# Performance work log

Hardware: AMD Instinct MI355X
Metric: run time of the kernel (lower is better)

## Reference

```python
import jax, jax.numpy as jnp
import numpy as np
import math

B, N, K = 16, 1024, 16
NODE_DIM, MSG = 32, 128
EDGE_DIM = 4
EIN = MSG + EDGE_DIM  # edge_input_dim = message_dim + edge_dim
EPS = 1e-8
PI = math.pi


def _knn(pts, k):
    # pairwise_distance_etaphi + topk(smallest) -> neighbor indices [B,N,K]
    eta, phi = pts[:, 0], pts[:, 1]                                  # [B,N]
    deta = eta[:, :, None] - eta[:, None, :]
    dphi = jnp.mod(phi[:, :, None] - phi[:, None, :] + PI, 2 * PI) - PI
    dist = deta ** 2 + dphi ** 2                                     # [B,N,N]
    _, idx = jax.lax.top_k(-dist, k)                                 # smallest-k, sorted
    return idx


def _gather(x, idx):
    # x: [B,C,N], idx: [B,N,K] -> neighbor features [B,C,N,K]
    return jnp.take_along_axis(x[:, :, None, :], idx[:, None, :, :], axis=3)


def _ptrapphi(x):
    px, py, pz, e = x[:, 0:1], x[:, 1:2], x[:, 2:3], x[:, 3:4]
    pt = jnp.sqrt(px ** 2 + py ** 2)
    rap = 0.5 * jnp.log1p(2.0 * pz / jnp.clip(e - pz, 1e-20))
    phi = jnp.arctan2(py, px)
    return pt, rap, phi


def _pairwise_lv_fts(xi, xj):
    # [lnkt, lnz, lndelta, lnm2] along channel dim
    pti, rapi, phii = _ptrapphi(xi)
    ptj, rapj, phij = _ptrapphi(xj)
    ptmin = jnp.minimum(pti, ptj)
    dphi = jnp.mod(phii - phij + PI, 2 * PI) - PI
    delta = jnp.sqrt((rapi - rapj) ** 2 + dphi ** 2)
    lndelta = jnp.log(jnp.clip(delta, EPS))
    lnkt = jnp.log(jnp.clip(ptmin * delta, EPS))
    lnz = jnp.log(jnp.clip(ptmin / jnp.clip(pti + ptj, EPS), EPS))
    xij = xi + xj
    m2 = jnp.clip(xij[:, 3:4] ** 2 - (xij[:, :3] ** 2).sum(1, keepdims=True), EPS)
    lnm2 = jnp.log(m2)
    return jnp.concatenate([lnkt, lnz, lndelta, lnm2], axis=1)


def _bn(x, s, b):
    # eval-mode BatchNorm folded into per-channel scale/bias
    sh = (1, -1) + (1,) * (x.ndim - 2)
    return x * s.reshape(sh) + b.reshape(sh)


def _conv1x1(w, x):
    return jnp.einsum('oc,bc...->bo...', w, x)


def setup_inputs():
    key = jax.random.key(0)
    ks = jax.random.split(key, 12)
    pts = jax.random.normal(ks[0], (B, 2, N), jnp.float32)
    fts = jax.random.normal(ks[1], (B, NODE_DIM, N), jnp.float32)
    p3 = jax.random.normal(ks[2], (B, 3, N), jnp.float32) * 5.0
    e = jnp.sqrt((p3 ** 2).sum(1, keepdims=True) + 0.5)  # physical 4-vectors (E > |p|)
    lvs = jnp.concatenate([p3, e], axis=1)
    mask = jax.random.bernoulli(ks[3], 0.9, (B, 1, N))
    w = lambda k, o, i: (jax.random.normal(k, (o, i), jnp.float32) / np.sqrt(i)).astype(jnp.float32)
    return dict(
        pts=pts, fts=fts, lvs=lvs, mask=mask,
        bn1_s=jnp.ones(NODE_DIM, jnp.float32), bn1_b=jnp.zeros(NODE_DIM, jnp.float32),
        w_node=w(ks[4], MSG // 2, NODE_DIM),
        bn2_s=jnp.ones(EIN, jnp.float32), bn2_b=jnp.zeros(EIN, jnp.float32),
        w_e1=w(ks[5], MSG, EIN),
        bn3_s=jnp.ones(MSG, jnp.float32), bn3_b=jnp.zeros(MSG, jnp.float32),
        w_e2=w(ks[6], MSG, MSG),
        se_w1=w(ks[7], MSG // 16, MSG),
        se_w2=w(ks[8], MSG, MSG // 16),
    )


def reference(pts, fts, lvs, mask, bn1_s, bn1_b, w_node, bn2_s, bn2_b, w_e1, bn3_s, bn3_b, w_e2, se_w1, se_w2):
    idx = _knn(pts, K)                                                  # [B,N,K]
    # node_encode: BN -> ReLU -> 1x1 conv (node_dim -> MSG//2)
    node = _conv1x1(w_node, jax.nn.relu(_bn(fts, bn1_s, bn1_b)))        # [B,MSG/2,N]
    node_ngb = _gather(node, idx)                                       # [B,MSG/2,N,K]
    node_ctr = jnp.broadcast_to(node[..., None], node_ngb.shape)
    lvs_ngb = _gather(lvs, idx)                                         # [B,4,N,K]
    lv_fts = _pairwise_lv_fts(jnp.broadcast_to(lvs[..., None], lvs_ngb.shape), lvs_ngb)
    mf = mask.astype(jnp.float32)
    valid = _gather(mf, idx) * mf[..., None]                            # [B,1,N,K]
    x = jnp.concatenate([node_ctr, node_ngb, lv_fts], axis=1)           # [B,EIN,N,K]
    # edge_mlp: BN-ReLU-Conv1x1 x2
    x = _conv1x1(w_e1, jax.nn.relu(_bn(x, bn2_s, bn2_b)))
    x = _conv1x1(w_e2, jax.nn.relu(_bn(x, bn3_s, bn3_b)))               # [B,MSG,N,K]
    # SqueezeAndExcitation2d over valid edges
    n = valid.sum((2, 3))
    n = jnp.where(n == 0, 1.0, n)                                       # [B,1]
    y = (x * valid).sum((2, 3)) / n                                     # [B,MSG]
    y = jax.nn.sigmoid(jax.nn.relu(y @ se_w1.T) @ se_w2.T)
    x = x * y[:, :, None, None]
    # masked mean aggregation over neighbors
    x = x * valid
    agg = x.sum(-1) / jnp.clip(valid.sum(-1), 1.0)                      # [B,MSG,N]
    return agg
```

## Files before the change

kernel.cpp:

```cpp
#include <hip/hip_runtime.h>
#include <hip/hip_bf16.h>
#include <math.h>

typedef unsigned short u16;
typedef unsigned long long u64;

#define BB 16
#define NN 1024
#define KK 16
#define MSG 128
#define EINC 132
#define EPSF 1e-8f
#define PIF 3.14159274101257324f
#define TWOPIF 6.28318548202514648f

__device__ __forceinline__ float bf2f(u16 u) {
    return __uint_as_float(((unsigned int)u) << 16);
}
__device__ __forceinline__ float ldf(const void* p, int i, int fdt) {
    return fdt ? ((const float*)p)[i] : bf2f(((const u16*)p)[i]);
}
__device__ __forceinline__ float4 ldf4(const void* p, int i, int fdt) {
    if (fdt) return ((const float4*)p)[i >> 2];
    ushort4 u = ((const ushort4*)p)[i >> 2];
    return make_float4(bf2f(u.x), bf2f(u.y), bf2f(u.z), bf2f(u.w));
}
__device__ __forceinline__ float maskval(const void* m, int i, int mode) {
    if (mode == 0) return bf2f(((const u16*)m)[i]);
    if (mode == 1) return ((const float*)m)[i];
    if (mode == 2) return ((const unsigned char*)m)[i] ? 1.f : 0.f;
    return ((const int*)m)[i] ? 1.f : 0.f;
}

__global__ void sniff_kernel(const unsigned int* __restrict__ bn1s,
                             const u16* __restrict__ mask,
                             int* __restrict__ ctl) {
    if (threadIdx.x == 0 && blockIdx.x == 0) {
        ctl[0] = (bn1s[0] == 0x3F800000u) ? 1 : 0;
        bool bf = false, f32 = false, i8 = false;
        for (int q = 0; q < 64; ++q) {
            u16 u = mask[q];
            if (u == 0x3F80u) { if ((q & 1) == 0) bf = true; else f32 = true; }
            if (u == 0x0101u) i8 = true;
        }
        ctl[1] = bf ? 0 : (f32 ? 1 : (i8 ? 2 : 3));
    }
}

__device__ __forceinline__ float wrap2pi(float dp) {
    if (dp >= TWOPIF) dp = __fsub_rn(dp, TWOPIF);
    if (dp < 0.f) dp = __fadd_rn(dp, TWOPIF);
    return dp;
}

__device__ __forceinline__ void sort16(u64* x) {
#pragma unroll
    for (int k = 2; k <= 16; k <<= 1)
#pragma unroll
        for (int j = k >> 1; j > 0; j >>= 1)
#pragma unroll
            for (int i = 0; i < 16; ++i) {
                int l = i ^ j;
                if (l > i) {
                    bool up = ((i & k) == 0);
                    bool lt = x[l] < x[i];
                    bool sw = up ? lt : !lt;
                    u64 a = sw ? x[l] : x[i];
                    u64 b = sw ? x[i] : x[l];
                    x[i] = a; x[l] = b;
                }
            }
}

__device__ __forceinline__ void merge16(u64* L, const u64* R) {
#pragma unroll
    for (int k = 0; k < 16; ++k) {
        u64 o = R[15 - k];
        L[k] = (o < L[k]) ? o : L[k];
    }
#pragma unroll
    for (int j = 8; j > 0; j >>= 1)
#pragma unroll
        for (int i = 0; i < 16; ++i) {
            int l = i ^ j;
            if (l > i) {
                bool sw = L[l] < L[i];
                u64 a = sw ? L[l] : L[i];
                u64 b = sw ? L[i] : L[l];
                L[i] = a; L[l] = b;
            }
        }
}

__global__ __launch_bounds__(256) void knn_kernel(const void* __restrict__ pts,
                                                  int* __restrict__ idx,
                                                  const int* __restrict__ ctl) {
    __shared__ __align__(16) char smem[24672];
    float* seL = (float*)smem;
    float* spL = seL + 1092;
    float* pdL = (float*)smem;
    u16*   piL = (u16*)(smem + 16448);
    int fdt = ctl[0];
    int blk = blockIdx.x;
    int b = blk >> 6;
    int ibase = (blk & 63) << 4;
    int t = threadIdx.x;
    int pb = b * 2 * NN;
    for (int j = t; j < NN; j += 256) {
        int a = (j >> 6) * 68 + (j & 63);
        seL[a] = ldf(pts, pb + j, fdt);
        spL[a] = ldf(pts, pb + NN + j, fdt);
    }
    __syncthreads();
    int p = t >> 4, s = t & 15;
    u64 lst[16];
    {
        int i = ibase + p;
        int ia = (i >> 6) * 68 + (i & 63);
        float ei = seL[ia], pii = spL[ia];
        u64 grp[16];
#pragma unroll
        for (int g = 0; g < 4; ++g) {
            const float* sep = &seL[s * 68 + g * 16];
            const float* spp = &spL[s * 68 + g * 16];
            int jb = (s << 6) + (g << 4);
#pragma unroll
            for (int q4 = 0; q4 < 4; ++q4) {
                float4 e4 = *(const float4*)(sep + 4 * q4);
                float4 p4 = *(const float4*)(spp + 4 * q4);
                float ee[4] = { e4.x, e4.y, e4.z, e4.w };
                float pp[4] = { p4.x, p4.y, p4.z, p4.w };
#pragma unroll
                for (int q = 0; q < 4; ++q) {
                    float de = __fsub_rn(ei, ee[q]);
                    float dp = wrap2pi(__fadd_rn(__fsub_rn(pii, pp[q]), PIF));
                    float dphi = __fsub_rn(dp, PIF);
                    float cd = __fadd_rn(__fmul_rn(de, de), __fmul_rn(dphi, dphi));
                    grp[q4 * 4 + q] = ((u64)__float_as_uint(cd) << 10)
                                      | (unsigned)(jb + q4 * 4 + q);
                }
            }
            sort16(grp);
            if (g == 0) {
#pragma unroll
                for (int k = 0; k < 16; ++k) lst[k] = grp[k];
            } else {
                merge16(lst, grp);
            }
        }
    }
    __syncthreads();
    {
        int base = p * 257 + s * 16;
#pragma unroll
        for (int k = 0; k < 16; ++k) {
            pdL[base + k] = __uint_as_float((unsigned)(lst[k] >> 10));
            piL[base + k] = (u16)(lst[k] & 1023u);
        }
    }
    for (int stg = 0; stg < 4; ++stg) {
        __syncthreads();
        int stride = 8 >> stg;
        if (s < stride) {
            int Lb = p * 257 + s * 16;
            int Rb = p * 257 + (s + stride) * 16;
            u64 L[16], R[16];
#pragma unroll
            for (int k = 0; k < 16; ++k)
                L[k] = ((u64)__float_as_uint(pdL[Lb + k]) << 10) | piL[Lb + k];
#pragma unroll
            for (int k = 0; k < 16; ++k)
                R[k] = ((u64)__float_as_uint(pdL[Rb + k]) << 10) | piL[Rb + k];
            merge16(L, R);
#pragma unroll
            for (int k = 0; k < 16; ++k) {
                pdL[Lb + k] = __uint_as_float((unsigned)(L[k] >> 10));
                piL[Lb + k] = (u16)(L[k] & 1023u);
            }
        }
    }
    __syncthreads();
    {
        int p2 = t >> 4, k2 = t & 15;
        idx[(b * NN + ibase + p2) * KK + k2] = (int)piL[p2 * 257 + k2];
    }
}

__global__ __launch_bounds__(256) void ab1_kernel(
    const void* __restrict__ fts, const void* __restrict__ lvs,
    const void* __restrict__ bn1_s, const void* __restrict__ bn1_b,
    const void* __restrict__ w_node,
    const void* __restrict__ bn2_s, const void* __restrict__ bn2_b,
    float* __restrict__ rAB, float* __restrict__ prpx,
    const int* __restrict__ ctl) {
    __shared__ __align__(16) float fL[32 * 36];
    __shared__ __align__(16) float wnL[64 * 36];
    __shared__ float s2L[128], b2L[128];
    int fdt = ctl[0];
    int blk = blockIdx.x;
    int b = blk >> 5;
    int ibase = (blk & 31) << 5;
    int t = threadIdx.x;
    {
        int c = t >> 3, q = t & 7;
        float s1c = ldf(bn1_s, c, fdt), b1c = ldf(bn1_b, c, fdt);
        float4 v = ldf4(fts, (b * 32 + c) * NN + ibase + q * 4, fdt);
        float vv[4] = { v.x, v.y, v.z, v.w };
#pragma unroll
        for (int j = 0; j < 4; ++j)
            fL[(q * 4 + j) * 36 + c] = fmaxf(vv[j] * s1c + b1c, 0.f);
    }
#pragma unroll
    for (int m = 0; m < 2; ++m) {
        int e = t * 2 + m;
        int o = e >> 3, q = e & 7;
        float4 w = ldf4(w_node, o * 32 + q * 4, fdt);
        float* d = &wnL[o * 36 + q * 4];
        d[0] = w.x; d[1] = w.y; d[2] = w.z; d[3] = w.w;
    }
    if (t < 128) { s2L[t] = ldf(bn2_s, t, fdt); b2L[t] = ldf(bn2_b, t, fdt); }
    if (t < 32) {
        int i = ibase + t;
        int lb = b * 4 * NN;
        float px = ldf(lvs, lb + i, fdt),          py = ldf(lvs, lb + NN + i, fdt);
        float pz = ldf(lvs, lb + 2 * NN + i, fdt), e  = ldf(lvs, lb + 3 * NN + i, fdt);
        float pt = sqrtf(px * px + py * py);
        float rr = 2.f * pz / fmaxf(e - pz, 1e-20f);
        rr = fmaxf(rr, -0.99999994f);
        float rap = 0.5f * log1pf(rr);
        float phi = atan2f(py, px);
        float* o = prpx + (size_t)(b * NN + i) * 8;
        o[0] = px; o[1] = py; o[2] = pz; o[3] = e;
        o[4] = pt; o[5] = rap; o[6] = phi; o[7] = 0.f;
    }
    __syncthreads();
    int p = t >> 3, og = t & 7;
    float fr[32];
#pragma unroll
    for (int cc = 0; cc < 32; cc += 4) {
        float4 v = *(const float4*)&fL[p * 36 + cc];
        fr[cc] = v.x; fr[cc + 1] = v.y; fr[cc + 2] = v.z; fr[cc + 3] = v.w;
    }
    float aa[8];
#pragma unroll
    for (int m = 0; m < 8; ++m) {
        int no = og * 8 + m;
        float a = 0.f;
#pragma unroll
        for (int cc = 0; cc < 32; cc += 4) {
            float4 w = *(const float4*)&wnL[no * 36 + cc];
            a += w.x * fr[cc] + w.y * fr[cc + 1] + w.z * fr[cc + 2] + w.w * fr[cc + 3];
        }
        aa[m] = a;
    }
    size_t base = (size_t)(b * NN + ibase + p) * 128 + og * 8;
    float lo[8], hi[8];
#pragma unroll
    for (int m = 0; m < 8; ++m) {
        int no = og * 8 + m;
        lo[m] = fmaxf(aa[m] * s2L[no] + b2L[no], 0.f);
        hi[m] = fmaxf(aa[m] * s2L[64 + no] + b2L[64 + no], 0.f);
    }
    *(float4*)(rAB + base)      = make_float4(lo[0], lo[1], lo[2], lo[3]);
    *(float4*)(rAB + base + 4)  = make_float4(lo[4], lo[5], lo[6], lo[7]);
    *(float4*)(rAB + base + 64) = make_float4(hi[0], hi[1], hi[2], hi[3]);
    *(float4*)(rAB + base + 68) = make_float4(hi[4], hi[5], hi[6], hi[7]);
}

__global__ __launch_bounds__(256) void ab2_kernel(
    const float* __restrict__ rAB, const void* __restrict__ w_e1,
    float* __restrict__ A, float* __restrict__ Bv,
    const int* __restrict__ ctl) {
    __shared__ float rT[64 * 68];
    __shared__ float wsh[2048];
    int fdt = ctl[0];
    int blk = blockIdx.x;
    int half = blk & 1;
    int pc = blk >> 1;
    int b = pc >> 4, i0 = (pc & 15) << 6;
    int t = threadIdx.x;
    {
        int r = t >> 2, q = t & 3;
        const float4* src = (const float4*)(rAB + (size_t)(b * NN + i0 + r) * 128
                                            + half * 64 + q * 16);
#pragma unroll
        for (int m = 0; m < 4; ++m) {
            float4 v = src[m];
            int c = q * 16 + 4 * m;
            rT[(c + 0) * 68 + r] = v.x; rT[(c + 1) * 68 + r] = v.y;
            rT[(c + 2) * 68 + r] = v.z; rT[(c + 3) * 68 + r] = v.w;
        }
    }
    float acc[8][4];
#pragma unroll
    for (int oi = 0; oi < 8; ++oi)
#pragma unroll
        for (int ci = 0; ci < 4; ++ci) acc[oi][ci] = 0.f;
    int og = t >> 4, cg = t & 15;
    for (int jt = 0; jt < 4; ++jt) {
        __syncthreads();
        {
            int o = t >> 1, jh = (t & 1) * 8;
            float4 wa = ldf4(w_e1, o * EINC + half * 64 + jt * 16 + jh, fdt);
            float4 wb = ldf4(w_e1, o * EINC + half * 64 + jt * 16 + jh + 4, fdt);
            wsh[(jh + 0) * 128 + o] = wa.x; wsh[(jh + 1) * 128 + o] = wa.y;
            wsh[(jh + 2) * 128 + o] = wa.z; wsh[(jh + 3) * 128 + o] = wa.w;
            wsh[(jh + 4) * 128 + o] = wb.x; wsh[(jh + 5) * 128 + o] = wb.y;
            wsh[(jh + 6) * 128 + o] = wb.z; wsh[(jh + 7) * 128 + o] = wb.w;
        }
        __syncthreads();
#pragma unroll
        for (int jj = 0; jj < 16; ++jj) {
            int c = jt * 16 + jj;
            float4 hv = *(const float4*)&rT[c * 68 + cg * 4];
            float4 w0 = *(const float4*)&wsh[jj * 128 + og * 8];
            float4 w1 = *(const float4*)&wsh[jj * 128 + og * 8 + 4];
            float wv[8] = { w0.x, w0.y, w0.z, w0.w, w1.x, w1.y, w1.z, w1.w };
            float hvv[4] = { hv.x, hv.y, hv.z, hv.w };
#pragma unroll
            for (int oi = 0; oi < 8; ++oi)
#pragma unroll
                for (int ci = 0; ci < 4; ++ci)
                    acc[oi][ci] += wv[oi] * hvv[ci];
        }
    }
    float* dst = half ? Bv : A;
#pragma unroll
    for (int ci = 0; ci < 4; ++ci) {
        size_t g = (size_t)(b * NN + i0 + cg * 4 + ci) * 128 + og * 8;
        *(float4*)(dst + g)     = make_float4(acc[0][ci], acc[1][ci], acc[2][ci], acc[3][ci]);
        *(float4*)(dst + g + 4) = make_float4(acc[4][ci], acc[5][ci], acc[6][ci], acc[7][ci]);
    }
}

__global__ __launch_bounds__(256) void edge_kernel(
    const void* __restrict__ mask, const int* __restrict__ idx,
    const float* __restrict__ A, const float* __restrict__ Bv,
    const float* __restrict__ prpx,
    const void* __restrict__ bn2_s, const void* __restrict__ bn2_b,
    const void* __restrict__ w_e1,
    const void* __restrict__ bn3_s, const void* __restrict__ bn3_b,
    float* __restrict__ Hs, float* __restrict__ cnt, float* __restrict__ Thp,
    const int* __restrict__ ctl) {
    __shared__ float rlvL[128 * 4];
    __shared__ float validL[128];
    __shared__ int   idxsL[128];
    __shared__ float thL[128 * 5];
    int fdt = ctl[0], mmode = ctl[1];
    int blk = blockIdx.x;
    int b = blk >> 7;
    int pbase = (blk & 127) << 3;
    int t = threadIdx.x;

    if (t < 128) {
        int col = t, pt = col >> 4, k = col & 15;
        int i = pbase + pt;
        int jn = idx[(b * NN + i) * KK + k];
        idxsL[col] = jn;
        float mi = maskval(mask, b * NN + i, mmode);
        float mj = maskval(mask, b * NN + jn, mmode);
        validL[col] = (mi != 0.f && mj != 0.f) ? 1.f : 0.f;
        const float4* pc = (const float4*)(prpx + (size_t)(b * NN + i) * 8);
        const float4* pn = (const float4*)(prpx + (size_t)(b * NN + jn) * 8);
        float4 c0 = pc[0], c1 = pc[1], n0 = pn[0], n1 = pn[1];
        float ptmin = fminf(c1.x, n1.x);
        float dpr = (c1.z - n1.z) + PIF;
        float r = fmodf(dpr, TWOPIF);
        r = (r < 0.f) ? r + TWOPIF : r;
        float dphi = r - PIF;
        float dr = c1.y - n1.y;
        float delta = sqrtf(dr * dr + dphi * dphi);
        float lndelta = logf(fmaxf(delta, EPSF));
        float lnkt = logf(fmaxf(ptmin * delta, EPSF));
        float lnz = logf(fmaxf(ptmin / fmaxf(c1.x + n1.x, EPSF), EPSF));
        float sx = c0.x + n0.x, sy = c0.y + n0.y, sz = c0.z + n0.z, see = c0.w + n0.w;
        float m2 = fmaxf(see * see - (sx * sx + sy * sy + sz * sz), EPSF);
        float f4a[4] = { lnkt, lnz, lndelta, logf(m2) };
        float rv[4];
#pragma unroll
        for (int q = 0; q < 4; ++q)
            rv[q] = fmaxf(f4a[q] * ldf(bn2_s, MSG + q, fdt) + ldf(bn2_b, MSG + q, fdt), 0.f);
        *(float4*)&rlvL[col * 4] = make_float4(rv[0], rv[1], rv[2], rv[3]);
    }
    __syncthreads();
    int pt = t >> 5, cq = t & 31;
    int i = pbase + pt;
    int c0 = cq * 4;
    float4 a4 = *(const float4*)(A + (size_t)(b * NN + i) * 128 + c0);
    float4 s3 = ldf4(bn3_s, c0, fdt), b3 = ldf4(bn3_b, c0, fdt);
    float4 w0 = ldf4(w_e1, (c0 + 0) * EINC + 128, fdt);
    float4 w1 = ldf4(w_e1, (c0 + 1) * EINC + 128, fdt);
    float4 w2 = ldf4(w_e1, (c0 + 2) * EINC + 128, fdt);
    float4 w3 = ldf4(w_e1, (c0 + 3) * EINC + 128, fdt);
    float4 acc = make_float4(0.f, 0.f, 0.f, 0.f);
#pragma unroll
    for (int k = 0; k < 16; ++k) {
        int col = pt * 16 + k;
        int jn = idxsL[col];
        float vk = validL[col];
        float4 rl = *(const float4*)&rlvL[col * 4];
        float4 b4 = *(const float4*)(Bv + (size_t)(b * NN + jn) * 128 + c0);
        float e0 = a4.x + b4.x + w0.x * rl.x + w0.y * rl.y + w0.z * rl.z + w0.w * rl.w;
        float e1 = a4.y + b4.y + w1.x * rl.x + w1.y * rl.y + w1.z * rl.z + w1.w * rl.w;
        float e2 = a4.z + b4.z + w2.x * rl.x + w2.y * rl.y + w2.z * rl.z + w2.w * rl.w;
        float e3 = a4.w + b4.w + w3.x * rl.x + w3.y * rl.y + w3.z * rl.z + w3.w * rl.w;
        acc.x += vk * fmaxf(s3.x * e0 + b3.x, 0.f);
        acc.y += vk * fmaxf(s3.y * e1 + b3.y, 0.f);
        acc.z += vk * fmaxf(s3.z * e2 + b3.z, 0.f);
        acc.w += vk * fmaxf(s3.w * e3 + b3.w, 0.f);
    }
    *(float4*)(Hs + (size_t)(b * NN + i) * 128 + c0) = acc;
    float4 a2;
    a2.x = acc.x + __shfl_down(acc.x, 32, 64);
    a2.y = acc.y + __shfl_down(acc.y, 32, 64);
    a2.z = acc.z + __shfl_down(acc.z, 32, 64);
    a2.w = acc.w + __shfl_down(acc.w, 32, 64);
    int wv_ = t >> 6;
    if ((t & 63) < 32) {
        thL[(cq * 4 + 0) * 5 + wv_] = a2.x;
        thL[(cq * 4 + 1) * 5 + wv_] = a2.y;
        thL[(cq * 4 + 2) * 5 + wv_] = a2.z;
        thL[(cq * 4 + 3) * 5 + wv_] = a2.w;
    }
    if (t < 8) {
        float cs = 0.f;
#pragma unroll
        for (int k = 0; k < 16; ++k) cs += validL[t * 16 + k];
        cnt[b * NN + pbase + t] = cs;
    }
    __syncthreads();
    if (t < 128)
        Thp[(size_t)blk * 128 + t] = thL[t * 5 + 0] + thL[t * 5 + 1]
                                   + thL[t * 5 + 2] + thL[t * 5 + 3];
}

__global__ __launch_bounds__(128) void se_kernel(const float* __restrict__ Thp,
                                                 const float* __restrict__ cnt,
                                                 const void* __restrict__ w_e2,
                                                 const void* __restrict__ se_w1,
                                                 const void* __restrict__ se_w2,
                                                 float* __restrict__ y,
                                                 const int* __restrict__ ctl) {
    int b = blockIdx.x, t = threadIdx.x;
    int fdt = ctl[0];
    __shared__ float ThL[128], ybar[MSG], hh[8], part[2];
    float a = 0.f;
    for (int m = t; m < NN; m += 128) a += cnt[b * NN + m];
#pragma unroll
    for (int off = 32; off; off >>= 1) a += __shfl_down(a, off, 64);
    if ((t & 63) == 0) part[t >> 6] = a;
    float tv = 0.f;
    for (int p = 0; p < 128; ++p) tv += Thp[(size_t)(b * 128 + p) * 128 + t];
    ThL[t] = tv;
    __syncthreads();
    float n = part[0] + part[1];
    n = (n == 0.f) ? 1.f : n;
    float T = 0.f;
#pragma unroll
    for (int j4 = 0; j4 < 32; ++j4) {
        float4 w = ldf4(w_e2, t * MSG + j4 * 4, fdt);
        T += w.x * ThL[j4 * 4] + w.y * ThL[j4 * 4 + 1] +
             w.z * ThL[j4 * 4 + 2] + w.w * ThL[j4 * 4 + 3];
    }
    ybar[t] = T / n;
    __syncthreads();
    if (t < 8) {
        float s = 0.f;
        for (int c = 0; c < MSG; ++c) s += ybar[c] * ldf(se_w1, t * MSG + c, fdt);
        hh[t] = fmaxf(s, 0.f);
    }
    __syncthreads();
    float s = 0.f;
#pragma unroll
    for (int j = 0; j < 8; ++j) s += hh[j] * ldf(se_w2, t * 8 + j, fdt);
    y[b * MSG + t] = 1.f / (1.f + expf(-s));
}

__global__ __launch_bounds__(256) void fin_kernel(const float* __restrict__ Hs,
                                                  const float* __restrict__ cnt,
                                                  const float* __restrict__ y,
                                                  const void* __restrict__ w_e2,
                                                  void* __restrict__ out,
                                                  const int* __restrict__ ctl) {
    __shared__ float HsT[128 * 68];
    __shared__ float wsh[16 * 64];
    __shared__ float yL[64], icL[64];
    int fdt = ctl[0];
    int blk = blockIdx.x;
    int oh = blk & 1;
    int pc = blk >> 1;
    int b = pc >> 4, i0 = (pc & 15) << 6;
    int t = threadIdx.x;
    {
        int r = t >> 2, q4 = t & 3;
        const float4* src = (const float4*)(Hs + (size_t)(b * NN + i0 + r) * 128 + q4 * 32);
#pragma unroll
        for (int m = 0; m < 8; ++m) {
            float4 v = src[m];
            int j = q4 * 32 + 4 * m;
            HsT[(j + 0) * 68 + r] = v.x; HsT[(j + 1) * 68 + r] = v.y;
            HsT[(j + 2) * 68 + r] = v.z; HsT[(j + 3) * 68 + r] = v.w;
        }
    }
    if (t < 64) yL[t] = y[b * 128 + oh * 64 + t];
    else if (t < 128) icL[t - 64] = 1.f / fmaxf(cnt[b * NN + i0 + (t - 64)], 1.f);
    float acc[4][4];
#pragma unroll
    for (int oi = 0; oi < 4; ++oi)
#pragma unroll
        for (int ci = 0; ci < 4; ++ci) acc[oi][ci] = 0.f;
    int og = t >> 4, cg = t & 15;
    for (int jt = 0; jt < 8; ++jt) {
        __syncthreads();
        {
            int o = t >> 2, jh = (t & 3) * 4;
            float4 wa = ldf4(w_e2, (oh * 64 + o) * MSG + jt * 16 + jh, fdt);
            wsh[(jh + 0) * 64 + o] = wa.x; wsh[(jh + 1) * 64 + o] = wa.y;
            wsh[(jh + 2) * 64 + o] = wa.z; wsh[(jh + 3) * 64 + o] = wa.w;
        }
        __syncthreads();
#pragma unroll
        for (int jj = 0; jj < 16; ++jj) {
            int j = jt * 16 + jj;
            float4 hv = *(const float4*)&HsT[j * 68 + cg * 4];
            float4 wv = *(const float4*)&wsh[jj * 64 + og * 4];
            float wvv[4] = { wv.x, wv.y, wv.z, wv.w };
            float hvv[4] = { hv.x, hv.y, hv.z, hv.w };
#pragma unroll
            for (int oi = 0; oi < 4; ++oi)
#pragma unroll
                for (int ci = 0; ci < 4; ++ci)
                    acc[oi][ci] += wvv[oi] * hvv[ci];
        }
    }
    float ic[4] = { icL[cg * 4], icL[cg * 4 + 1], icL[cg * 4 + 2], icL[cg * 4 + 3] };
#pragma unroll
    for (int oi = 0; oi < 4; ++oi) {
        int o = oh * 64 + og * 4 + oi;
        float yv = yL[og * 4 + oi];
        float4 r;
        r.x = acc[oi][0] * yv * ic[0];
        r.y = acc[oi][1] * yv * ic[1];
        r.z = acc[oi][2] * yv * ic[2];
        r.w = acc[oi][3] * yv * ic[3];
        size_t g = (size_t)(b * 128 + o) * 1024 + i0 + cg * 4;
        if (fdt) *(float4*)((float*)out + g) = r;
        else {
            __hip_bfloat16* ob = (__hip_bfloat16*)out + g;
            ob[0] = __float2bfloat16(r.x); ob[1] = __float2bfloat16(r.y);
            ob[2] = __float2bfloat16(r.z); ob[3] = __float2bfloat16(r.w);
        }
    }
}

extern "C" void kernel_launch(void* const* d_in, const int* in_sizes, int n_in,
                              void* d_out, int out_size, void* d_ws, size_t ws_size,
                              hipStream_t stream) {
    const void* pts   = d_in[0];
    const void* fts   = d_in[1];
    const void* lvs   = d_in[2];
    const void* mask  = d_in[3];
    const void* bn1_s = d_in[4];
    const void* bn1_b = d_in[5];
    const void* w_node= d_in[6];
    const void* bn2_s = d_in[7];
    const void* bn2_b = d_in[8];
    const void* w_e1  = d_in[9];
    const void* bn3_s = d_in[10];
    const void* bn3_b = d_in[11];
    const void* w_e2  = d_in[12];
    const void* se_w1 = d_in[13];
    const void* se_w2 = d_in[14];

    char* ws = (char*)d_ws;
    size_t off = 0;
    int*   idx   = (int*)(ws + off);   off += (size_t)BB * NN * KK * 4;
    float* A     = (float*)(ws + off); off += (size_t)BB * NN * 128 * 4;
    float* Bv    = (float*)(ws + off); off += (size_t)BB * NN * 128 * 4;
    float* prpx  = (float*)(ws + off); off += (size_t)BB * NN * 8 * 4;
    float* HsU   = (float*)(ws + off); off += (size_t)BB * NN * 128 * 4;
    float* cnt   = (float*)(ws + off); off += (size_t)BB * NN * 4;
    float* Thp   = (float*)(ws + off); off += (size_t)2048 * 128 * 4;
    float* y     = (float*)(ws + off); off += (size_t)BB * 128 * 4;
    int*   ctl   = (int*)(ws + off);

    sniff_kernel<<<1, 64, 0, stream>>>((const unsigned int*)bn1_s, (const u16*)mask, ctl);
    knn_kernel<<<1024, 256, 0, stream>>>(pts, idx, ctl);
    ab1_kernel<<<512, 256, 0, stream>>>(fts, lvs, bn1_s, bn1_b, w_node,
                                        bn2_s, bn2_b, HsU, prpx, ctl);
    ab2_kernel<<<512, 256, 0, stream>>>(HsU, w_e1, A, Bv, ctl);
    edge_kernel<<<2048, 256, 0, stream>>>(mask, idx, A, Bv, prpx, bn2_s, bn2_b,
                                          w_e1, bn3_s, bn3_b, HsU, cnt, Thp, ctl);
    se_kernel<<<BB, 128, 0, stream>>>(Thp, cnt, w_e2, se_w1, se_w2, y, ctl);
    fin_kernel<<<512, 256, 0, stream>>>(HsU, cnt, y, w_e2, d_out, ctl);
}
```

Before: 208.8 us.

## Split kNN over more blocks and parallelize SE partial-sum reduction

The kNN kernel now handles 8 query points per block, with 32 threads per point each scanning 32 candidates, instead of 16 points per block with 16 threads each scanning 64. This doubles the block count and adds one merge stage. The serial 128-step per-thread reduction of Thp inside the 16-block SE kernel moves into a new 256-block reduction kernel using shuffles. This adds a launch and a small buffer but removes a long serial loop that ran on only 16 blocks.

```diff
diff --git a/kernel.cpp b/kernel.cpp
--- a/kernel.cpp
+++ b/kernel.cpp
@@ -95,15 +95,15 @@
 __global__ __launch_bounds__(256) void knn_kernel(const void* __restrict__ pts,
                                                   int* __restrict__ idx,
                                                   const int* __restrict__ ctl) {
-    __shared__ __align__(16) char smem[24672];
+    __shared__ __align__(16) char smem[24960];
     float* seL = (float*)smem;
     float* spL = seL + 1092;
     float* pdL = (float*)smem;
-    u16*   piL = (u16*)(smem + 16448);
+    u16*   piL = (u16*)(smem + 16640);
     int fdt = ctl[0];
     int blk = blockIdx.x;
-    int b = blk >> 6;
-    int ibase = (blk & 63) << 4;
+    int b = blk >> 7;
+    int ibase = (blk & 127) << 3;
     int t = threadIdx.x;
     int pb = b * 2 * NN;
     for (int j = t; j < NN; j += 256) {
@@ -112,7 +112,7 @@
         spL[a] = ldf(pts, pb + NN + j, fdt);
     }
     __syncthreads();
-    int p = t >> 4, s = t & 15;
+    int p = t >> 5, s = t & 31;
     u64 lst[16];
     {
         int i = ibase + p;
@@ -120,10 +120,11 @@
         float ei = seL[ia], pii = spL[ia];
         u64 grp[16];
 #pragma unroll
-        for (int g = 0; g < 4; ++g) {
-            const float* sep = &seL[s * 68 + g * 16];
-            const float* spp = &spL[s * 68 + g * 16];
-            int jb = (s << 6) + (g << 4);
+        for (int g = 0; g < 2; ++g) {
+            int ab = (s >> 1) * 68 + (s & 1) * 32 + g * 16;
+            const float* sep = &seL[ab];
+            const float* spp = &spL[ab];
+            int jb = (s << 5) + (g << 4);
 #pragma unroll
             for (int q4 = 0; q4 < 4; ++q4) {
                 float4 e4 = *(const float4*)(sep + 4 * q4);
@@ -151,19 +152,19 @@
     }
     __syncthreads();
     {
-        int base = p * 257 + s * 16;
+        int base = p * 520 + s * 16;
 #pragma unroll
         for (int k = 0; k < 16; ++k) {
             pdL[base + k] = __uint_as_float((unsigned)(lst[k] >> 10));
             piL[base + k] = (u16)(lst[k] & 1023u);
         }
     }
-    for (int stg = 0; stg < 4; ++stg) {
+    for (int stg = 0; stg < 5; ++stg) {
         __syncthreads();
-        int stride = 8 >> stg;
+        int stride = 16 >> stg;
         if (s < stride) {
-            int Lb = p * 257 + s * 16;
-            int Rb = p * 257 + (s + stride) * 16;
+            int Lb = p * 520 + s * 16;
+            int Rb = p * 520 + (s + stride) * 16;
             u64 L[16], R[16];
 #pragma unroll
             for (int k = 0; k < 16; ++k)
@@ -180,9 +181,9 @@
         }
     }
     __syncthreads();
-    {
+    if (t < 128) {
         int p2 = t >> 4, k2 = t & 15;
-        idx[(b * NN + ibase + p2) * KK + k2] = (int)piL[p2 * 257 + k2];
+        idx[(b * NN + ibase + p2) * KK + k2] = (int)piL[p2 * 520 + k2];
     }
 }
 
@@ -434,7 +435,28 @@
                                    + thL[t * 5 + 2] + thL[t * 5 + 3];
 }
 
-__global__ __launch_bounds__(128) void se_kernel(const float* __restrict__ Thp,
+__global__ __launch_bounds__(256) void thred_kernel(const float* __restrict__ Thp,
+                                                    float* __restrict__ Th) {
+    int blk = blockIdx.x;
+    int b = blk >> 4, cg = blk & 15;
+    int t = threadIdx.x;
+    int p = t >> 3, ch = t & 7;
+    int c = cg * 8 + ch;
+    float a = 0.f;
+#pragma unroll
+    for (int q = 0; q < 4; ++q)
+        a += Thp[(size_t)(b * 128 + p + q * 32) * 128 + c];
+    a += __shfl_down(a, 32, 64);
+    a += __shfl_down(a, 16, 64);
+    a += __shfl_down(a, 8, 64);
+    __shared__ float part[4][8];
+    if ((t & 63) < 8) part[t >> 6][t & 7] = a;
+    __syncthreads();
+    if (t < 8) Th[b * 128 + cg * 8 + t] =
+        part[0][t] + part[1][t] + part[2][t] + part[3][t];
+}
+
+__global__ __launch_bounds__(128) void se_kernel(const float* __restrict__ Th,
                                                  const float* __restrict__ cnt,
                                                  const void* __restrict__ w_e2,
                                                  const void* __restrict__ se_w1,
@@ -449,9 +471,7 @@
 #pragma unroll
     for (int off = 32; off; off >>= 1) a += __shfl_down(a, off, 64);
     if ((t & 63) == 0) part[t >> 6] = a;
-    float tv = 0.f;
-    for (int p = 0; p < 128; ++p) tv += Thp[(size_t)(b * 128 + p) * 128 + t];
-    ThL[t] = tv;
+    ThL[t] = Th[b * 128 + t];
     __syncthreads();
     float n = part[0] + part[1];
     n = (n == 0.f) ? 1.f : n;
@@ -581,16 +601,18 @@
     float* HsU   = (float*)(ws + off); off += (size_t)BB * NN * 128 * 4;
     float* cnt   = (float*)(ws + off); off += (size_t)BB * NN * 4;
     float* Thp   = (float*)(ws + off); off += (size_t)2048 * 128 * 4;
+    float* Th    = (float*)(ws + off); off += (size_t)BB * 128 * 4;
     float* y     = (float*)(ws + off); off += (size_t)BB * 128 * 4;
     int*   ctl   = (int*)(ws + off);
 
     sniff_kernel<<<1, 64, 0, stream>>>((const unsigned int*)bn1_s, (const u16*)mask, ctl);
-    knn_kernel<<<1024, 256, 0, stream>>>(pts, idx, ctl);
+    knn_kernel<<<2048, 256, 0, stream>>>(pts, idx, ctl);
     ab1_kernel<<<512, 256, 0, stream>>>(fts, lvs, bn1_s, bn1_b, w_node,
                                         bn2_s, bn2_b, HsU, prpx, ctl);
     ab2_kernel<<<512, 256, 0, stream>>>(HsU, w_e1, A, Bv, ctl);
     edge_kernel<<<2048, 256, 0, stream>>>(mask, idx, A, Bv, prpx, bn2_s, bn2_b,
                                           w_e1, bn3_s, bn3_b, HsU, cnt, Thp, ctl);
-    se_kernel<<<BB, 128, 0, stream>>>(Thp, cnt, w_e2, se_w1, se_w2, y, ctl);
+    thred_kernel<<<256, 256, 0, stream>>>(Thp, Th);
+    se_kernel<<<BB, 128, 0, stream>>>(Th, cnt, w_e2, se_w1, se_w2, y, ctl);
     fin_kernel<<<512, 256, 0, stream>>>(HsU, cnt, y, w_e2, d_out, ctl);
 }
```

New measurement: 225.6 us. 8.0% more time.
